# Kernel optimization log

Hardware: AMD Instinct MI355X
Metric: run time of the kernel (lower is better)

The kernel has to match this reference:

```python
import jax, jax.numpy as jnp
import numpy as np

HIDDEN = 1024
FEAT = 2048
BOTTLENECK = 512
B, T = 64, 512


def setup_inputs() -> dict:
    key = jax.random.key(0)
    k1, k2, k3, k4, k5 = jax.random.split(key, 5)
    hidden = jax.random.normal(k1, (B, HIDDEN), dtype=jnp.float32)
    feats = jax.random.normal(k2, (B, T, FEAT), dtype=jnp.float32)
    # nn.Linear weights stored as [out, in]; apply as x @ W.T
    W = jax.random.normal(k3, (BOTTLENECK, HIDDEN), dtype=jnp.float32) * (1.0 / np.sqrt(HIDDEN))
    U = jax.random.normal(k4, (BOTTLENECK, FEAT), dtype=jnp.float32) * (1.0 / np.sqrt(FEAT))
    b = jnp.ones((BOTTLENECK,), dtype=jnp.float32)
    w = jax.random.normal(k5, (1, BOTTLENECK), dtype=jnp.float32) * (1.0 / np.sqrt(BOTTLENECK))
    return {"hidden": hidden, "feats": feats, "W": W, "U": U, "b": b, "w": w}


def reference(hidden, feats, W, U, b, w):
    Wh = hidden @ W.T                      # [B, K]
    Uv = jnp.einsum('btf,kf->btk', feats, U)  # [B, T, K]
    e = jnp.tanh(Wh[:, None, :] + Uv + b)  # [B, T, K]
    energies = jnp.einsum('btk,ok->bto', e, w)  # [B, T, 1]
    weights = jax.nn.softmax(energies, axis=1)  # softmax over time
    attn_feats = jnp.sum(feats * weights, axis=1)  # [B, F]
    return attn_feats, weights
```

## Files before the change

kernel.cpp:

```cpp
#include <hip/hip_runtime.h>
#include <hip/hip_bf16.h>
#include <math.h>

#define BATCH 64
#define TDIM 512
#define FEAT 2048
#define HID 1024
#define KDIM 512
#define MROWS (BATCH * TDIM)

typedef __attribute__((ext_vector_type(8))) short short8;
typedef __attribute__((ext_vector_type(4))) float floatx4;

#define GLL16(g, l)                                                     \
    __builtin_amdgcn_global_load_lds(                                   \
        (const __attribute__((address_space(1))) void*)(g),             \
        (__attribute__((address_space(3))) void*)(l), 16, 0, 0)

__device__ __forceinline__ unsigned short f2bf(float x) {
    unsigned int u = __float_as_uint(x);
    u += 0x7FFFu + ((u >> 16) & 1u);
    return (unsigned short)(u >> 16);
}

__global__ __launch_bounds__(256) void k_convert(const float* __restrict__ src,
                                                 unsigned short* __restrict__ dst,
                                                 int n4) {
    int stride = gridDim.x * blockDim.x;
    for (int i = blockIdx.x * blockDim.x + threadIdx.x; i < n4; i += stride) {
        float4 v = ((const float4*)src)[i];
        ushort4 o;
        o.x = f2bf(v.x); o.y = f2bf(v.y); o.z = f2bf(v.z); o.w = f2bf(v.w);
        ((ushort4*)dst)[i] = o;
    }
}

__global__ __launch_bounds__(256) void k1_whb(const float* __restrict__ hidden,
                                              const float* __restrict__ W,
                                              const float* __restrict__ bias,
                                              float* __restrict__ whb) {
    int b = blockIdx.y;
    int k = blockIdx.x * 4 + (threadIdx.x >> 6);
    int lane = threadIdx.x & 63;
    const float* hrow = hidden + (size_t)b * HID;
    const float* wrow = W + (size_t)k * HID;
    float acc = 0.f;
    #pragma unroll 4
    for (int h = lane; h < HID; h += 64) acc += hrow[h] * wrow[h];
    #pragma unroll
    for (int off = 32; off > 0; off >>= 1) acc += __shfl_down(acc, off, 64);
    if (lane == 0) whb[b * KDIM + k] = acc + bias[k];
}

__global__ __launch_bounds__(256) void k2_mfma(const unsigned short* __restrict__ fB,
                                               const unsigned short* __restrict__ uB,
                                               const float* __restrict__ whb,
                                               const float* __restrict__ wvec,
                                               float* __restrict__ partial) {
    __shared__ unsigned short As[128 * 32];
    __shared__ unsigned short Bs[128 * 32];
    __shared__ float sums[2][128];

    const int tid  = threadIdx.x;
    const int wave = tid >> 6;
    const int lane = tid & 63;
    const int row0 = blockIdx.x * 128;
    const int k0   = blockIdx.y * 128;
    const int wm = wave >> 1, wn = wave & 1;
    const int col = lane & 15, quad = lane >> 4;

    const int c0 = wave * 128 + lane;
    const int c1 = c0 + 64;
    const unsigned short* gA0 = fB + (size_t)(row0 + (c0 >> 2)) * FEAT + (c0 & 3) * 8;
    const unsigned short* gA1 = fB + (size_t)(row0 + (c1 >> 2)) * FEAT + (c1 & 3) * 8;
    const unsigned short* gB0 = uB + (size_t)(k0 + (c0 >> 2)) * FEAT + (c0 & 3) * 8;
    const unsigned short* gB1 = uB + (size_t)(k0 + (c1 >> 2)) * FEAT + (c1 & 3) * 8;
    unsigned short* lA0 = As + wave * 1024;
    unsigned short* lA1 = lA0 + 512;
    unsigned short* lB0 = Bs + wave * 1024;
    unsigned short* lB1 = lB0 + 512;

    floatx4 acc[4][4];
    #pragma unroll
    for (int i = 0; i < 4; ++i)
        #pragma unroll
        for (int j = 0; j < 4; ++j) acc[i][j] = (floatx4){0.f, 0.f, 0.f, 0.f};

    for (int f0 = 0; f0 < FEAT; f0 += 32) {
        GLL16(gA0, lA0); GLL16(gA1, lA1);
        GLL16(gB0, lB0); GLL16(gB1, lB1);
        gA0 += 32; gA1 += 32; gB0 += 32; gB1 += 32;
        __syncthreads();

        short8 af[4], bf[4];
        #pragma unroll
        for (int i = 0; i < 4; ++i)
            af[i] = *(const short8*)&As[(wm * 64 + i * 16 + col) * 32 + quad * 8];
        #pragma unroll
        for (int j = 0; j < 4; ++j)
            bf[j] = *(const short8*)&Bs[(wn * 64 + j * 16 + col) * 32 + quad * 8];
        #pragma unroll
        for (int i = 0; i < 4; ++i)
            #pragma unroll
            for (int j = 0; j < 4; ++j)
                acc[i][j] = __builtin_amdgcn_mfma_f32_16x16x32_bf16(
                    af[i], bf[j], acc[i][j], 0, 0, 0);
        __syncthreads();
    }

    const int b = row0 >> 9;
    float wk[4], hk[4];
    #pragma unroll
    for (int j = 0; j < 4; ++j) {
        int k = k0 + wn * 64 + j * 16 + col;
        wk[j] = wvec[k];
        hk[j] = whb[b * KDIM + k];
    }
    #pragma unroll
    for (int i = 0; i < 4; ++i) {
        #pragma unroll
        for (int r = 0; r < 4; ++r) {
            float s = 0.f;
            #pragma unroll
            for (int j = 0; j < 4; ++j)
                s += tanhf(acc[i][j][r] + hk[j]) * wk[j];
            #pragma unroll
            for (int off = 8; off > 0; off >>= 1)
                s += __shfl_down(s, off, 16);
            if (col == 0)
                sums[wn][wm * 64 + i * 16 + quad * 4 + r] = s;
        }
    }
    __syncthreads();
    if (tid < 128)
        partial[blockIdx.y * MROWS + row0 + tid] = sums[0][tid] + sums[1][tid];
}

#define BM 128
#define BN 128
#define BF 16
#define LDSPAD 4

__global__ __launch_bounds__(256) void k2_energy(const float* __restrict__ feats,
                                                 const float* __restrict__ U,
                                                 const float* __restrict__ whb,
                                                 const float* __restrict__ wvec,
                                                 float* __restrict__ partial) {
    __shared__ __align__(16) float As[BF][BM + LDSPAD];
    __shared__ __align__(16) float Us[BF][BN + LDSPAD];

    const int row0 = blockIdx.x * BM;
    const int k0   = blockIdx.y * BN;
    const int tid  = threadIdx.x;
    const int tx   = tid & 15;
    const int ty   = tid >> 4;

    float acc[8][8];
    #pragma unroll
    for (int i = 0; i < 8; ++i)
        #pragma unroll
        for (int j = 0; j < 8; ++j) acc[i][j] = 0.f;

    for (int f0 = 0; f0 < FEAT; f0 += BF) {
        #pragma unroll
        for (int l = 0; l < 2; ++l) {
            int li = tid + l * 256;
            int r  = li >> 2;
            int c4 = (li & 3) * 4;
            float4 av = *(const float4*)(feats + (size_t)(row0 + r) * FEAT + f0 + c4);
            float4 uv = *(const float4*)(U     + (size_t)(k0   + r) * FEAT + f0 + c4);
            As[c4 + 0][r] = av.x; As[c4 + 1][r] = av.y;
            As[c4 + 2][r] = av.z; As[c4 + 3][r] = av.w;
            Us[c4 + 0][r] = uv.x; Us[c4 + 1][r] = uv.y;
            Us[c4 + 2][r] = uv.z; Us[c4 + 3][r] = uv.w;
        }
        __syncthreads();
        #pragma unroll
        for (int kf = 0; kf < BF; ++kf) {
            float4 a0 = *(const float4*)&As[kf][ty * 8];
            float4 a1 = *(const float4*)&As[kf][ty * 8 + 4];
            float4 u0 = *(const float4*)&Us[kf][tx * 8];
            float4 u1 = *(const float4*)&Us[kf][tx * 8 + 4];
            float a[8] = {a0.x, a0.y, a0.z, a0.w, a1.x, a1.y, a1.z, a1.w};
            float u[8] = {u0.x, u0.y, u0.z, u0.w, u1.x, u1.y, u1.z, u1.w};
            #pragma unroll
            for (int i = 0; i < 8; ++i)
                #pragma unroll
                for (int j = 0; j < 8; ++j) acc[i][j] += a[i] * u[j];
        }
        __syncthreads();
    }

    const int b = row0 >> 9;
    float psum[8];
    #pragma unroll
    for (int i = 0; i < 8; ++i) {
        float s = 0.f;
        #pragma unroll
        for (int j = 0; j < 8; ++j) {
            int k = k0 + tx * 8 + j;
            s += tanhf(acc[i][j] + whb[b * KDIM + k]) * wvec[k];
        }
        psum[i] = s;
    }
    #pragma unroll
    for (int off = 8; off > 0; off >>= 1)
        #pragma unroll
        for (int i = 0; i < 8; ++i) psum[i] += __shfl_down(psum[i], off, 16);

    if (tx == 0) {
        int c = blockIdx.y;
        #pragma unroll
        for (int i = 0; i < 8; ++i)
            partial[c * MROWS + row0 + ty * 8 + i] = psum[i];
    }
}

__global__ __launch_bounds__(512) void k3_softmax(const float* __restrict__ partial,
                                                  float* __restrict__ wout) {
    int b = blockIdx.x;
    int t = threadIdx.x;
    float e = 0.f;
    #pragma unroll
    for (int c = 0; c < 4; ++c) e += partial[c * MROWS + b * TDIM + t];

    __shared__ float sm[512];
    sm[t] = e;
    __syncthreads();
    #pragma unroll
    for (int s = 256; s > 0; s >>= 1) {
        if (t < s) sm[t] = fmaxf(sm[t], sm[t + s]);
        __syncthreads();
    }
    float m = sm[0];
    __syncthreads();
    float ex = __expf(e - m);
    sm[t] = ex;
    __syncthreads();
    #pragma unroll
    for (int s = 256; s > 0; s >>= 1) {
        if (t < s) sm[t] += sm[t + s];
        __syncthreads();
    }
    float inv = 1.f / sm[0];
    wout[b * TDIM + t] = ex * inv;
}

__global__ __launch_bounds__(256) void k4_pool(const float* __restrict__ feats,
                                               const float* __restrict__ weights,
                                               float* __restrict__ out) {
    int b = blockIdx.y;
    int f4 = (blockIdx.x * 256 + threadIdx.x) * 4;
    __shared__ float wsm[TDIM];
    wsm[threadIdx.x]       = weights[b * TDIM + threadIdx.x];
    wsm[threadIdx.x + 256] = weights[b * TDIM + 256 + threadIdx.x];
    __syncthreads();

    const float* fp = feats + (size_t)b * TDIM * FEAT + f4;
    float ax = 0.f, ay = 0.f, az = 0.f, aw = 0.f;
    float bx = 0.f, by = 0.f, bz = 0.f, bw = 0.f;
    for (int t = 0; t < TDIM; t += 4) {
        float4 v0 = *(const float4*)(fp + (size_t)(t + 0) * FEAT);
        float4 v1 = *(const float4*)(fp + (size_t)(t + 1) * FEAT);
        float4 v2 = *(const float4*)(fp + (size_t)(t + 2) * FEAT);
        float4 v3 = *(const float4*)(fp + (size_t)(t + 3) * FEAT);
        float w0 = wsm[t], w1 = wsm[t + 1], w2 = wsm[t + 2], w3 = wsm[t + 3];
        ax += v0.x * w0; ay += v0.y * w0; az += v0.z * w0; aw += v0.w * w0;
        bx += v1.x * w1; by += v1.y * w1; bz += v1.z * w1; bw += v1.w * w1;
        ax += v2.x * w2; ay += v2.y * w2; az += v2.z * w2; aw += v2.w * w2;
        bx += v3.x * w3; by += v3.y * w3; bz += v3.z * w3; bw += v3.w * w3;
    }
    float4 o;
    o.x = ax + bx; o.y = ay + by; o.z = az + bz; o.w = aw + bw;
    *(float4*)(out + (size_t)b * FEAT + f4) = o;
}

extern "C" void kernel_launch(void* const* d_in, const int* in_sizes, int n_in,
                              void* d_out, int out_size, void* d_ws, size_t ws_size,
                              hipStream_t stream) {
    const float* hidden = (const float*)d_in[0];
    const float* feats  = (const float*)d_in[1];
    const float* W      = (const float*)d_in[2];
    const float* U      = (const float*)d_in[3];
    const float* bias   = (const float*)d_in[4];
    const float* wvec   = (const float*)d_in[5];

    float* out         = (float*)d_out;
    float* attn_out    = out;
    float* weights_out = out + (size_t)BATCH * FEAT;
    float* whb         = weights_out;
    float* partial     = attn_out;

    const size_t featsN = (size_t)MROWS * FEAT;
    const size_t uN     = (size_t)KDIM * FEAT;
    const bool bf16path = ws_size >= (featsN + uN) * sizeof(unsigned short);

    k1_whb<<<dim3(KDIM / 4, BATCH), 256, 0, stream>>>(hidden, W, bias, whb);

    if (bf16path) {
        unsigned short* fBf = (unsigned short*)d_ws;
        unsigned short* uBf = fBf + featsN;
        k_convert<<<1024, 256, 0, stream>>>(feats, fBf, (int)(featsN / 4));
        k_convert<<<256, 256, 0, stream>>>(U, uBf, (int)(uN / 4));
        k2_mfma<<<dim3(MROWS / 128, KDIM / 128), 256, 0, stream>>>(
            fBf, uBf, whb, wvec, partial);
    } else {
        k2_energy<<<dim3(MROWS / 128, KDIM / 128), 256, 0, stream>>>(
            feats, U, whb, wvec, partial);
    }

    k3_softmax<<<dim3(BATCH), 512, 0, stream>>>(partial, weights_out);
    k4_pool<<<dim3(FEAT / 1024, BATCH), 256, 0, stream>>>(feats, weights_out, attn_out);
}
```

Before: 560.6 us.

## Split attention pooling across time chunks and swizzle LDS in MFMA GEMM

```diff
diff --git a/kernel.cpp b/kernel.cpp
--- a/kernel.cpp
+++ b/kernel.cpp
@@ -8,6 +8,8 @@
 #define HID 1024
 #define KDIM 512
 #define MROWS (BATCH * TDIM)
+#define TCH 8
+#define TCLEN (TDIM / TCH)
 
 typedef __attribute__((ext_vector_type(8))) short short8;
 typedef __attribute__((ext_vector_type(4))) float floatx4;
@@ -71,15 +73,20 @@
 
     const int c0 = wave * 128 + lane;
     const int c1 = c0 + 64;
-    const unsigned short* gA0 = fB + (size_t)(row0 + (c0 >> 2)) * FEAT + (c0 & 3) * 8;
-    const unsigned short* gA1 = fB + (size_t)(row0 + (c1 >> 2)) * FEAT + (c1 & 3) * 8;
-    const unsigned short* gB0 = uB + (size_t)(k0 + (c0 >> 2)) * FEAT + (c0 & 3) * 8;
-    const unsigned short* gB1 = uB + (size_t)(k0 + (c1 >> 2)) * FEAT + (c1 & 3) * 8;
+    const int r0c = c0 >> 2, r1c = c1 >> 2;
+    const int q0 = (c0 & 3) ^ ((r0c >> 1) & 3);
+    const int q1 = (c1 & 3) ^ ((r1c >> 1) & 3);
+    const unsigned short* gA0 = fB + (size_t)(row0 + r0c) * FEAT + q0 * 8;
+    const unsigned short* gA1 = fB + (size_t)(row0 + r1c) * FEAT + q1 * 8;
+    const unsigned short* gB0 = uB + (size_t)(k0 + r0c) * FEAT + q0 * 8;
+    const unsigned short* gB1 = uB + (size_t)(k0 + r1c) * FEAT + q1 * 8;
     unsigned short* lA0 = As + wave * 1024;
     unsigned short* lA1 = lA0 + 512;
     unsigned short* lB0 = Bs + wave * 1024;
     unsigned short* lB1 = lB0 + 512;
 
+    const int sw = (quad ^ ((col >> 1) & 3)) * 8;
+
     floatx4 acc[4][4];
     #pragma unroll
     for (int i = 0; i < 4; ++i)
@@ -95,10 +102,10 @@
         short8 af[4], bf[4];
         #pragma unroll
         for (int i = 0; i < 4; ++i)
-            af[i] = *(const short8*)&As[(wm * 64 + i * 16 + col) * 32 + quad * 8];
+            af[i] = *(const short8*)&As[(wm * 64 + i * 16 + col) * 32 + sw];
         #pragma unroll
         for (int j = 0; j < 4; ++j)
-            bf[j] = *(const short8*)&Bs[(wn * 64 + j * 16 + col) * 32 + quad * 8];
+            bf[j] = *(const short8*)&Bs[(wn * 64 + j * 16 + col) * 32 + sw];
         #pragma unroll
         for (int i = 0; i < 4; ++i)
             #pragma unroll
@@ -246,20 +253,21 @@
     wout[b * TDIM + t] = ex * inv;
 }
 
-__global__ __launch_bounds__(256) void k4_pool(const float* __restrict__ feats,
-                                               const float* __restrict__ weights,
-                                               float* __restrict__ out) {
-    int b = blockIdx.y;
+__global__ __launch_bounds__(256) void k4_partial(const float* __restrict__ feats,
+                                                  const float* __restrict__ weights,
+                                                  float* __restrict__ partial4) {
+    int b  = blockIdx.z;
+    int t0 = blockIdx.y * TCLEN;
     int f4 = (blockIdx.x * 256 + threadIdx.x) * 4;
-    __shared__ float wsm[TDIM];
-    wsm[threadIdx.x]       = weights[b * TDIM + threadIdx.x];
-    wsm[threadIdx.x + 256] = weights[b * TDIM + 256 + threadIdx.x];
-    __syncthreads();
-
-    const float* fp = feats + (size_t)b * TDIM * FEAT + f4;
+    __shared__ float wsm[TCLEN];
+    if (threadIdx.x < TCLEN) wsm[threadIdx.x] = weights[b * TDIM + t0 + threadIdx.x];
+    __syncthreads();
+
+    const float* fp = feats + (size_t)b * TDIM * FEAT + (size_t)t0 * FEAT + f4;
     float ax = 0.f, ay = 0.f, az = 0.f, aw = 0.f;
     float bx = 0.f, by = 0.f, bz = 0.f, bw = 0.f;
-    for (int t = 0; t < TDIM; t += 4) {
+    #pragma unroll 4
+    for (int t = 0; t < TCLEN; t += 4) {
         float4 v0 = *(const float4*)(fp + (size_t)(t + 0) * FEAT);
         float4 v1 = *(const float4*)(fp + (size_t)(t + 1) * FEAT);
         float4 v2 = *(const float4*)(fp + (size_t)(t + 2) * FEAT);
@@ -272,6 +280,39 @@
     }
     float4 o;
     o.x = ax + bx; o.y = ay + by; o.z = az + bz; o.w = aw + bw;
+    *(float4*)(partial4 + ((size_t)blockIdx.y * BATCH + b) * FEAT + f4) = o;
+}
+
+__global__ __launch_bounds__(256) void k5_reduce(const float* __restrict__ partial4,
+                                                 float* __restrict__ out) {
+    int i4 = blockIdx.x * 256 + threadIdx.x;
+    float4 s = ((const float4*)partial4)[i4];
+    #pragma unroll
+    for (int c = 1; c < TCH; ++c) {
+        float4 v = ((const float4*)partial4)[(size_t)c * (BATCH * FEAT / 4) + i4];
+        s.x += v.x; s.y += v.y; s.z += v.z; s.w += v.w;
+    }
+    ((float4*)out)[i4] = s;
+}
+
+__global__ __launch_bounds__(256) void k4_direct(const float* __restrict__ feats,
+                                                 const float* __restrict__ weights,
+                                                 float* __restrict__ out) {
+    int b = blockIdx.y;
+    int f4 = (blockIdx.x * 256 + threadIdx.x) * 4;
+    __shared__ float wsm[TDIM];
+    wsm[threadIdx.x]       = weights[b * TDIM + threadIdx.x];
+    wsm[threadIdx.x + 256] = weights[b * TDIM + 256 + threadIdx.x];
+    __syncthreads();
+
+    const float* fp = feats + (size_t)b * TDIM * FEAT + f4;
+    float ax = 0.f, ay = 0.f, az = 0.f, aw = 0.f;
+    for (int t = 0; t < TDIM; ++t) {
+        float4 v = *(const float4*)(fp + (size_t)t * FEAT);
+        float w = wsm[t];
+        ax += v.x * w; ay += v.y * w; az += v.z * w; aw += v.w * w;
+    }
+    float4 o = {ax, ay, az, aw};
     *(float4*)(out + (size_t)b * FEAT + f4) = o;
 }
 
@@ -293,22 +334,29 @@
 
     const size_t featsN = (size_t)MROWS * FEAT;
     const size_t uN     = (size_t)KDIM * FEAT;
-    const bool bf16path = ws_size >= (featsN + uN) * sizeof(unsigned short);
+    const size_t bf16Bytes = (featsN + uN) * sizeof(unsigned short);
+    const size_t poolBytes = (size_t)TCH * BATCH * FEAT * sizeof(float);
+    const bool fast = ws_size >= bf16Bytes + poolBytes;
 
     k1_whb<<<dim3(KDIM / 4, BATCH), 256, 0, stream>>>(hidden, W, bias, whb);
 
-    if (bf16path) {
+    if (fast) {
         unsigned short* fBf = (unsigned short*)d_ws;
         unsigned short* uBf = fBf + featsN;
+        float* pool4 = (float*)((char*)d_ws + bf16Bytes);
         k_convert<<<1024, 256, 0, stream>>>(feats, fBf, (int)(featsN / 4));
         k_convert<<<256, 256, 0, stream>>>(U, uBf, (int)(uN / 4));
         k2_mfma<<<dim3(MROWS / 128, KDIM / 128), 256, 0, stream>>>(
             fBf, uBf, whb, wvec, partial);
+        k3_softmax<<<dim3(BATCH), 512, 0, stream>>>(partial, weights_out);
+        k4_partial<<<dim3(FEAT / 1024, TCH, BATCH), 256, 0, stream>>>(
+            feats, weights_out, pool4);
+        k5_reduce<<<dim3(BATCH * FEAT / 4 / 256), 256, 0, stream>>>(pool4, attn_out);
     } else {
         k2_energy<<<dim3(MROWS / 128, KDIM / 128), 256, 0, stream>>>(
             feats, U, whb, wvec, partial);
-    }
-
-    k3_softmax<<<dim3(BATCH), 512, 0, stream>>>(partial, weights_out);
-    k4_pool<<<dim3(FEAT / 1024, BATCH), 256, 0, stream>>>(feats, weights_out, attn_out);
-}
+        k3_softmax<<<dim3(BATCH), 512, 0, stream>>>(partial, weights_out);
+        k4_direct<<<dim3(FEAT / 1024, BATCH), 256, 0, stream>>>(
+            feats, weights_out, attn_out);
+    }
+}
```

New measurement: 555.2 us. No clear change (-1.0%).
